# Kernel tuning notes

Measured on AMD Instinct MI355X. Metric: run time of the kernel, lower is better.

## Reference

```python
import jax, jax.numpy as jnp
import numpy as np
from functools import partial

M, K, N = 256, 32, 2048
TOL = 1e-6


def _masked_solve(AtA, Atb, P):
    # Solve (A^T A)[P,P] z_P = (A^T b)[P], zeros elsewhere, via a masked k x k system.
    Pm = P.astype(AtA.dtype)
    Msys = AtA * (Pm[:, None] * Pm[None, :]) + jnp.diag(1.0 - Pm)
    z = jnp.linalg.solve(Msys, Atb * Pm)
    return z * Pm


def _nnls_col(AtA, Atb):
    # fnnls active-set NNLS for one column: argmin_{s>=0} ||x - A s||^2
    k = Atb.shape[0]
    max_it = 3 * k

    def inner_cond(st):
        P, s, z, it = st
        return jnp.logical_and(jnp.any(jnp.logical_and(P, z <= TOL)), it < max_it)

    def inner_body(st):
        P, s, z, it = st
        mask = jnp.logical_and(P, z <= TOL)
        denom = s - z
        ratio = jnp.where(mask, s / jnp.where(denom != 0, denom, 1.0), jnp.inf)
        alpha = jnp.min(ratio)
        s = s + alpha * (z - s)
        P = jnp.logical_and(P, s > TOL)
        s = jnp.where(P, s, 0.0)
        z = _masked_solve(AtA, Atb, P)
        return (P, s, z, it + 1)

    def outer_cond(st):
        P, s, it = st
        w = Atb - AtA @ s
        return jnp.logical_and(jnp.any(jnp.logical_and(~P, w > TOL)), it < max_it)

    def outer_body(st):
        P, s, it = st
        w = jnp.where(P, -jnp.inf, Atb - AtA @ s)
        j = jnp.argmax(w)
        P = P.at[j].set(True)
        z = _masked_solve(AtA, Atb, P)
        P, s, z, _ = jax.lax.while_loop(inner_cond, inner_body, (P, s, z, jnp.int32(0)))
        s = jnp.where(P, z, 0.0)
        return (P, s, it + 1)

    P0 = jnp.zeros(k, dtype=bool)
    s0 = jnp.zeros(k, dtype=Atb.dtype)
    _, s, _ = jax.lax.while_loop(outer_cond, outer_body, (P0, s0, jnp.int32(0)))
    return s


def setup_inputs() -> dict:
    key = jax.random.key(0)
    kx, ka = jax.random.split(key)
    X = jax.random.uniform(kx, (M, N), dtype=jnp.float32)  # nonneg data matrix
    A = jnp.abs(jax.random.normal(ka, (M, K), dtype=jnp.float32))  # module's A init
    return {"input": X, "A": A}


def reference(input, A):
    # S = q(X, A): column-wise nonneg least squares, batched over the n columns.
    AtA = A.T @ A            # [k,k]
    AtX = A.T @ input        # [k,n]
    S = jax.vmap(_nnls_col, in_axes=(None, 1), out_axes=1)(AtA, AtX)  # [k,n]
    return S
```

## Files before the change

kernel.cpp:

```cpp
#include <hip/hip_runtime.h>
#include <math.h>

#define KDIM 32
#define MDIM 256
#define NDIM 2048
#define W_TOL 1e-3f

__device__ __forceinline__ float lane_bcast(float x, int lane) {
  return __int_as_float(__builtin_amdgcn_readlane(__float_as_int(x), lane));
}
__device__ __forceinline__ float rcp_newton(float x) {
  float r;
  asm("v_rcp_f32 %0, %1" : "=v"(r) : "v"(x));
  r = r * (2.0f - x * r);
  return r;
}
__device__ __forceinline__ float rcp_fast(float x) {
  float r;
  asm("v_rcp_f32 %0, %1" : "=v"(r) : "v"(x));
  return r;
}

__global__ __launch_bounds__(256) void prep_kernel(const float* __restrict__ A,
                                                   const float* __restrict__ X,
                                                   float* __restrict__ AtA,
                                                   float* __restrict__ Ainv,
                                                   float* __restrict__ AtXt) {
  __shared__ float buf[8448];
  const int t = threadIdx.x;
  {
    const float4* A4 = reinterpret_cast<const float4*>(A);
    float4* B4 = reinterpret_cast<float4*>(buf);
#pragma unroll
    for (int i = 0; i < 8; ++i) B4[t + 256 * i] = A4[t + 256 * i];
  }
  __syncthreads();

  if (blockIdx.x < 64) {
    const int nl = t & 31;
    const int ch = t >> 5;
    const int n = blockIdx.x * 32 + nl;
    float acc[KDIM];
#pragma unroll
    for (int k = 0; k < KDIM; ++k) acc[k] = 0.f;
#pragma unroll 4
    for (int mm = 0; mm < 32; ++mm) {
      const int m = ch * 32 + mm;
      const float x = X[m * NDIM + n];
#pragma unroll
      for (int qq = 0; qq < 8; ++qq) {
        const float4 a4 = *reinterpret_cast<const float4*>(&buf[m * KDIM + qq * 4]);
        acc[4 * qq + 0] = fmaf(a4.x, x, acc[4 * qq + 0]);
        acc[4 * qq + 1] = fmaf(a4.y, x, acc[4 * qq + 1]);
        acc[4 * qq + 2] = fmaf(a4.z, x, acc[4 * qq + 2]);
        acc[4 * qq + 3] = fmaf(a4.w, x, acc[4 * qq + 3]);
      }
    }
    __syncthreads();
#pragma unroll
    for (int k = 0; k < KDIM; ++k) buf[ch * 1056 + nl * 33 + k] = acc[k];
    __syncthreads();
    float v[4];
#pragma unroll
    for (int q = 0; q < 4; ++q) {
      const int f = t * 4 + q, kk = f & 31, nn = f >> 5;
      float s = 0.f;
#pragma unroll
      for (int g = 0; g < 8; ++g) s += buf[g * 1056 + nn * 33 + kk];
      v[q] = s;
    }
    const float4 o = {v[0], v[1], v[2], v[3]};
    reinterpret_cast<float4*>(AtXt + blockIdx.x * 32 * KDIM)[t] = o;
  } else {
    const int i = t >> 3, j0 = (t & 7) * 4;
    float a0 = 0.f, a1 = 0.f, a2 = 0.f, a3 = 0.f;
    for (int m = 0; m < MDIM; ++m) {
      const float ai = buf[m * KDIM + i];
      const float4 vj = *reinterpret_cast<const float4*>(&buf[m * KDIM + j0]);
      a0 = fmaf(ai, vj.x, a0);
      a1 = fmaf(ai, vj.y, a1);
      a2 = fmaf(ai, vj.z, a2);
      a3 = fmaf(ai, vj.w, a3);
    }
    __syncthreads();
    {
      const float4 o = {a0, a1, a2, a3};
      reinterpret_cast<float4*>(AtA)[t] = o;
    }
    buf[i * 33 + j0 + 0] = a0;
    buf[i * 33 + j0 + 1] = a1;
    buf[i * 33 + j0 + 2] = a2;
    buf[i * 33 + j0 + 3] = a3;
    __syncthreads();
    if (t < 64) {
      const int r = t & 31;
      float m_[KDIM], g_[KDIM];
#pragma unroll
      for (int c = 0; c < KDIM; ++c) {
        m_[c] = buf[r * 33 + c];
        g_[c] = (r == c) ? 1.f : 0.f;
      }
      float myinv = 0.f;
#pragma unroll
      for (int j = 0; j < KDIM; ++j) {
        const float inv = rcp_newton(lane_bcast(m_[j], j));
        const float f = (r != j) ? m_[j] * inv : 0.f;
#pragma unroll
        for (int c = j + 1; c < KDIM; ++c) m_[c] = fmaf(-f, lane_bcast(m_[c], j), m_[c]);
#pragma unroll
        for (int c = 0; c < KDIM; ++c) g_[c] = fmaf(-f, lane_bcast(g_[c], j), g_[c]);
        if (r == j) myinv = inv;
      }
      if (t < 32) {
#pragma unroll
        for (int c = 0; c < KDIM; ++c) Ainv[r * KDIM + c] = myinv * g_[c];
      }
    }
  }
}

__global__ __launch_bounds__(64, 2) void nnls_kernel(const float* __restrict__ AtA_g,
                                                     const float* __restrict__ Ainv_g,
                                                     const float* __restrict__ AtXt,
                                                     float* __restrict__ S) {
  const int l = threadIdx.x;
  const int r = l & 31;
  const int n = blockIdx.x;

  const float atb = AtXt[n * KDIM + r];

  float ata[KDIM], g[KDIM];
#pragma unroll
  for (int q = 0; q < KDIM / 4; ++q) {
    const float4 v = reinterpret_cast<const float4*>(AtA_g + r * KDIM)[q];
    ata[4 * q + 0] = v.x; ata[4 * q + 1] = v.y; ata[4 * q + 2] = v.z; ata[4 * q + 3] = v.w;
    const float4 u = reinterpret_cast<const float4*>(Ainv_g + r * KDIM)[q];
    g[4 * q + 0] = u.x; g[4 * q + 1] = u.y; g[4 * q + 2] = u.z; g[4 * q + 3] = u.w;
  }

  float y;
  {
    float s0 = 0.f, s1 = 0.f, s2 = 0.f, s3 = 0.f;
#pragma unroll
    for (int c = 0; c < KDIM; c += 4) {
      s0 = fmaf(g[c + 0], lane_bcast(atb, c + 0), s0);
      s1 = fmaf(g[c + 1], lane_bcast(atb, c + 1), s1);
      s2 = fmaf(g[c + 2], lane_bcast(atb, c + 2), s2);
      s3 = fmaf(g[c + 3], lane_bcast(atb, c + 3), s3);
    }
    y = (s0 + s1) + (s2 + s3);
  }

  auto solve_dual = [&](unsigned int Pm) -> float {
    const unsigned int Rm = ~Pm;
    const int p = __popc(Pm);
    if (p <= 32 - p) {
      const bool actl = (Pm >> r) & 1u;
      float m[KDIM];
#pragma unroll
      for (int c = 0; c < KDIM; ++c)
        m[c] = (actl && ((Pm >> c) & 1u)) ? ata[c] : ((r == c) ? 1.f : 0.f);
      float rhs = actl ? atb : 0.f;
      float myinv = 0.f;
#pragma unroll
      for (int j = 0; j < KDIM; ++j) {
        if ((Pm >> j) & 1u) {
          const float inv = rcp_fast(lane_bcast(m[j], j));
          const float f = (r != j) ? m[j] * inv : 0.f;
#pragma unroll
          for (int c = j + 1; c < KDIM; ++c) m[c] = fmaf(-f, lane_bcast(m[c], j), m[c]);
          rhs = fmaf(-f, lane_bcast(rhs, j), rhs);
          if (r == j) myinv = inv;
        }
      }
      return rhs * myinv;
    } else {
      const bool reml = (Rm >> r) & 1u;
      float m[KDIM];
#pragma unroll
      for (int c = 0; c < KDIM; ++c)
        m[c] = (reml && ((Rm >> c) & 1u)) ? g[c] : ((r == c) ? 1.f : 0.f);
      float rhs = reml ? y : 0.f;
      float myinv = 0.f;
#pragma unroll
      for (int j = 0; j < KDIM; ++j) {
        if ((Rm >> j) & 1u) {
          const float inv = rcp_fast(lane_bcast(m[j], j));
          const float f = (r != j) ? m[j] * inv : 0.f;
#pragma unroll
          for (int c = j + 1; c < KDIM; ++c) m[c] = fmaf(-f, lane_bcast(m[c], j), m[c]);
          rhs = fmaf(-f, lane_bcast(rhs, j), rhs);
          if (r == j) myinv = inv;
        }
      }
      const float u = rhs * myinv;
      float z0 = y, z1 = 0.f, z2 = 0.f, z3 = 0.f;
#pragma unroll
      for (int c = 0; c < KDIM; c += 4) {
        z0 = fmaf(-g[c + 0], lane_bcast(u, c + 0), z0);
        z1 = fmaf(-g[c + 1], lane_bcast(u, c + 1), z1);
        z2 = fmaf(-g[c + 2], lane_bcast(u, c + 2), z2);
        z3 = fmaf(-g[c + 3], lane_bcast(u, c + 3), z3);
      }
      return (z0 + z1) + (z2 + z3);
    }
  };

  unsigned int P = (unsigned int)(__ballot(atb > 1e-6f) & 0xffffffffull);
  float z = (P == 0xffffffffu) ? y : solve_dual(P);

  float zeps = 0.f, weps = W_TOL;
  int best = 1000;
  bool conv = false;
  for (int it = 0; it < 8; ++it) {
    const bool act = (P >> r) & 1u;
    float s0 = 0.f, s1 = 0.f, s2 = 0.f, s3 = 0.f;
#pragma unroll
    for (int c = 0; c < KDIM; c += 4) {
      s0 = fmaf(ata[c + 0], lane_bcast(z, c + 0), s0);
      s1 = fmaf(ata[c + 1], lane_bcast(z, c + 1), s1);
      s2 = fmaf(ata[c + 2], lane_bcast(z, c + 2), s2);
      s3 = fmaf(ata[c + 3], lane_bcast(z, c + 3), s3);
    }
    const float w = atb - ((s0 + s1) + (s2 + s3));
    const bool pred = act ? (z < -zeps) : (w > weps);
    const unsigned int u = (unsigned int)(__ballot(pred) & 0xffffffffull);
    if (u == 0u) { conv = true; break; }
    const int ninf = __popc(u);
    if (ninf < best) {
      best = ninf;
    } else {
      zeps = fminf(zeps * 4.f + 2e-6f, 2.5e-4f);
      weps *= 4.f;
    }
    P = (P & ~(u & P)) | (u & ~P);
    z = solve_dual(P);
  }

  if (!conv) {
    const unsigned int drop =
        (unsigned int)(__ballot(((P >> r) & 1u) && (z < -2.5e-4f)) & 0xffffffffull);
    if (drop != 0u) {
      P &= ~drop;
      z = solve_dual(P);
    }
  }

  if (l < KDIM) S[r * NDIM + n] = ((P >> r) & 1u) ? fmaxf(z, 0.f) : 0.f;
}

extern "C" void kernel_launch(void* const* d_in, const int* in_sizes, int n_in,
                              void* d_out, int out_size, void* d_ws, size_t ws_size,
                              hipStream_t stream) {
  const float* X = (const float*)d_in[0];
  const float* A = (const float*)d_in[1];
  float* S = (float*)d_out;
  float* AtA = (float*)d_ws;
  float* Ainv = AtA + KDIM * KDIM;
  float* AtXt = Ainv + KDIM * KDIM;

  prep_kernel<<<65, 256, 0, stream>>>(A, X, AtA, Ainv, AtXt);
  nnls_kernel<<<NDIM, 64, 0, stream>>>(AtA, Ainv, AtXt, S);
}
```

Before: 32.65 us.

## Read A directly from global, prioritize solve waves, shortcut first all-active iteration

The prep kernel drops the LDS staging copy of A and its barriers, reading A rows straight from global/cache in both the AtX and AtA branches. The NNLS solve raises wave priority with s_setprio during the elimination so busy waves get issue preference. When every coefficient starts active, the first iteration skips the w = AtA*z matvec (w is zero for the unconstrained solution) and checks only for negative z. These cut redundant setup and per-column work, at the cost of more global loads in prep.

```diff
diff --git a/kernel.cpp b/kernel.cpp
--- a/kernel.cpp
+++ b/kernel.cpp
@@ -28,13 +28,6 @@
                                                    float* __restrict__ AtXt) {
   __shared__ float buf[8448];
   const int t = threadIdx.x;
-  {
-    const float4* A4 = reinterpret_cast<const float4*>(A);
-    float4* B4 = reinterpret_cast<float4*>(buf);
-#pragma unroll
-    for (int i = 0; i < 8; ++i) B4[t + 256 * i] = A4[t + 256 * i];
-  }
-  __syncthreads();
 
   if (blockIdx.x < 64) {
     const int nl = t & 31;
@@ -47,16 +40,16 @@
     for (int mm = 0; mm < 32; ++mm) {
       const int m = ch * 32 + mm;
       const float x = X[m * NDIM + n];
+      const float4* Arow = reinterpret_cast<const float4*>(A + m * KDIM);
 #pragma unroll
       for (int qq = 0; qq < 8; ++qq) {
-        const float4 a4 = *reinterpret_cast<const float4*>(&buf[m * KDIM + qq * 4]);
+        const float4 a4 = Arow[qq];
         acc[4 * qq + 0] = fmaf(a4.x, x, acc[4 * qq + 0]);
         acc[4 * qq + 1] = fmaf(a4.y, x, acc[4 * qq + 1]);
         acc[4 * qq + 2] = fmaf(a4.z, x, acc[4 * qq + 2]);
         acc[4 * qq + 3] = fmaf(a4.w, x, acc[4 * qq + 3]);
       }
     }
-    __syncthreads();
 #pragma unroll
     for (int k = 0; k < KDIM; ++k) buf[ch * 1056 + nl * 33 + k] = acc[k];
     __syncthreads();
@@ -75,14 +68,13 @@
     const int i = t >> 3, j0 = (t & 7) * 4;
     float a0 = 0.f, a1 = 0.f, a2 = 0.f, a3 = 0.f;
     for (int m = 0; m < MDIM; ++m) {
-      const float ai = buf[m * KDIM + i];
-      const float4 vj = *reinterpret_cast<const float4*>(&buf[m * KDIM + j0]);
+      const float ai = A[m * KDIM + i];
+      const float4 vj = *reinterpret_cast<const float4*>(A + m * KDIM + j0);
       a0 = fmaf(ai, vj.x, a0);
       a1 = fmaf(ai, vj.y, a1);
       a2 = fmaf(ai, vj.z, a2);
       a3 = fmaf(ai, vj.w, a3);
     }
-    __syncthreads();
     {
       const float4 o = {a0, a1, a2, a3};
       reinterpret_cast<float4*>(AtA)[t] = o;
@@ -152,8 +144,10 @@
   }
 
   auto solve_dual = [&](unsigned int Pm) -> float {
+    __builtin_amdgcn_s_setprio(1);
     const unsigned int Rm = ~Pm;
     const int p = __popc(Pm);
+    float zret;
     if (p <= 32 - p) {
       const bool actl = (Pm >> r) & 1u;
       float m[KDIM];
@@ -173,7 +167,7 @@
           if (r == j) myinv = inv;
         }
       }
-      return rhs * myinv;
+      zret = rhs * myinv;
     } else {
       const bool reml = (Rm >> r) & 1u;
       float m[KDIM];
@@ -202,17 +196,35 @@
         z2 = fmaf(-g[c + 2], lane_bcast(u, c + 2), z2);
         z3 = fmaf(-g[c + 3], lane_bcast(u, c + 3), z3);
       }
-      return (z0 + z1) + (z2 + z3);
-    }
+      zret = (z0 + z1) + (z2 + z3);
+    }
+    __builtin_amdgcn_s_setprio(0);
+    return zret;
   };
 
   unsigned int P = (unsigned int)(__ballot(atb > 1e-6f) & 0xffffffffull);
-  float z = (P == 0xffffffffu) ? y : solve_dual(P);
-
+  float z;
   float zeps = 0.f, weps = W_TOL;
   int best = 1000;
   bool conv = false;
-  for (int it = 0; it < 8; ++it) {
+  int it0;
+  if (P == 0xffffffffu) {
+    z = y;
+    const unsigned int u0 = (unsigned int)(__ballot(z < 0.f) & 0xffffffffull);
+    if (u0 == 0u) {
+      conv = true;
+    } else {
+      best = __popc(u0);
+      P &= ~u0;
+      z = solve_dual(P);
+    }
+    it0 = 1;
+  } else {
+    z = solve_dual(P);
+    it0 = 0;
+  }
+
+  for (int it = it0; it < 8 && !conv; ++it) {
     const bool act = (P >> r) & 1u;
     float s0 = 0.f, s1 = 0.f, s2 = 0.f, s3 = 0.f;
 #pragma unroll
```

Result: slower. 43.31 us (+32.6%).
